# Kernel tuning notes

Measured on AMD Instinct MI355X. Metric: run time of the kernel, lower is better.

Reference implementation:

```python
import jax, jax.numpy as jnp
import numpy as np

N_NODES = 50000
N_EDGES = 800000
N_GRAPHS = 64
HEADS = 4
IN_CH, HID_CH, OUT_CH = 128, 64, 32


def setup_inputs() -> dict:
    key = jax.random.key(0)
    ks = jax.random.split(key, 13)
    x = jax.random.normal(ks[0], (N_NODES, IN_CH), dtype=jnp.float32)
    edge_index = jax.random.randint(ks[1], (2, N_EDGES), 0, N_NODES, dtype=jnp.int64)
    tensor_batch = jnp.sort(jax.random.randint(ks[2], (N_NODES,), 0, N_GRAPHS, dtype=jnp.int64))
    s = 0.1
    return {
        "x": x,
        "edge_index": edge_index,
        "tensor_batch": tensor_batch,
        "W1": jax.random.normal(ks[3], (IN_CH, HEADS * HID_CH), dtype=jnp.float32) * s,
        "a_src1": jax.random.normal(ks[4], (HEADS, HID_CH), dtype=jnp.float32) * s,
        "a_dst1": jax.random.normal(ks[5], (HEADS, HID_CH), dtype=jnp.float32) * s,
        "b1": jnp.zeros((HEADS * HID_CH,), dtype=jnp.float32),
        "W2": jax.random.normal(ks[6], (HEADS * HID_CH, HEADS * OUT_CH), dtype=jnp.float32) * s,
        "a_src2": jax.random.normal(ks[7], (HEADS, OUT_CH), dtype=jnp.float32) * s,
        "a_dst2": jax.random.normal(ks[8], (HEADS, OUT_CH), dtype=jnp.float32) * s,
        "b2": jnp.zeros((HEADS * OUT_CH,), dtype=jnp.float32),
        "Wout": jax.random.normal(ks[9], (HEADS * OUT_CH, 2), dtype=jnp.float32) * s,
        "bout": jnp.zeros((2,), dtype=jnp.float32),
    }


def gat_conv(x, src, dst, W, a_src, a_dst, b, heads, ch):
    """PyG-style GATConv (eval mode, self-loops already appended)."""
    N = x.shape[0]
    h = (x @ W).reshape(N, heads, ch)            # [N,H,C] per-head projection
    s = jnp.sum(h * a_src, axis=-1)              # [N,H] source attention term
    d = jnp.sum(h * a_dst, axis=-1)              # [N,H] dest attention term
    e = jax.nn.leaky_relu(s[src] + d[dst], negative_slope=0.2)   # [E,H]
    # segment softmax over incoming edges of each destination node
    m = jax.ops.segment_max(e, dst, num_segments=N)              # [N,H]
    ex = jnp.exp(e - m[dst])
    denom = jax.ops.segment_sum(ex, dst, num_segments=N)         # [N,H]
    alpha = ex / (denom[dst] + 1e-16)                            # [E,H]
    out = jax.ops.segment_sum(h[src] * alpha[:, :, None], dst, num_segments=N)
    return out.reshape(N, heads * ch) + b


def reference(x, edge_index, tensor_batch, W1, a_src1, a_dst1, b1,
              W2, a_src2, a_dst2, b2, Wout, bout):
    N = x.shape[0]
    loop = jnp.arange(N, dtype=edge_index.dtype)
    src = jnp.concatenate([edge_index[0], loop])  # add self-loops (PyG default)
    dst = jnp.concatenate([edge_index[1], loop])
    h = jax.nn.relu(gat_conv(x, src, dst, W1, a_src1, a_dst1, b1, HEADS, HID_CH))
    h = jax.nn.relu(gat_conv(h, src, dst, W2, a_src2, a_dst2, b2, HEADS, OUT_CH))
    # global mean pool per graph
    sums = jax.ops.segment_sum(h, tensor_batch, num_segments=N_GRAPHS)
    counts = jax.ops.segment_sum(jnp.ones((N, 1), h.dtype), tensor_batch, num_segments=N_GRAPHS)
    pooled = sums / jnp.maximum(counts, 1.0)
    logits = pooled @ Wout + bout
    return jax.nn.softmax(logits, axis=-1)
```

## Files before the change

kernel.cpp:

```cpp
#include <hip/hip_runtime.h>
#include <hip/hip_bf16.h>

#define N_NODES 50000
#define N_EDGES 800000
#define N_GRAPHS 64
#define HEADS 4
#define IN_CH 128
#define HID 64
#define F1 256
#define OUT_CH 32
#define F2 128
#define POOL_SPLITS 16
#define SCAN_B 256
#define SCAN_NB ((N_NODES + SCAN_B - 1) / SCAN_B)
#define GEMM_GRID ((N_NODES + 63) / 64)
#define COUNT_GRID ((N_EDGES + 255) / 256)
#define SCATTER_GRID ((N_EDGES / 4 + 255) / 256)

typedef unsigned short ushortT;
typedef unsigned int uintT;
typedef short v8s __attribute__((ext_vector_type(8)));
typedef float v4f __attribute__((ext_vector_type(4)));
typedef float v2f __attribute__((ext_vector_type(2)));

__device__ __forceinline__ ushortT f2bf(float f) {
    union { float f; unsigned int i; } v; v.f = f;
    unsigned int x = v.i;
    unsigned int r = (x + 0x7fffu + ((x >> 16) & 1u)) >> 16;
    return (ushortT)r;
}
__device__ __forceinline__ float bf_lo(uintT w) {
    union { unsigned int i; float f; } v; v.i = w << 16; return v.f;
}
__device__ __forceinline__ float bf_hi(uintT w) {
    union { unsigned int i; float f; } v; v.i = w & 0xffff0000u; return v.f;
}
__device__ __forceinline__ unsigned char f2fp8(float f) {
    return (unsigned char)__builtin_amdgcn_cvt_pk_fp8_f32(f, f, 0u, false);
}
__device__ __forceinline__ void fp8x4_acc(uintT w, float ex, float* acc) {
    v2f p0 = __builtin_amdgcn_cvt_pk_f32_fp8(w, false);
    v2f p1 = __builtin_amdgcn_cvt_pk_f32_fp8(w, true);
    acc[0] += ex * p0.x; acc[1] += ex * p0.y;
    acc[2] += ex * p1.x; acc[3] += ex * p1.y;
}

__device__ __forceinline__ void packW_one(const float* __restrict__ W,
                                          uint4* __restrict__ dst,
                                          int i, int FIN, int FOUT) {
    int KC = FIN / 32;
    int lane = i & 63, g = i >> 6;
    int kc = g % KC, nt = g / KC;
    int n = nt * 16 + (lane & 15);
    int kbase = kc * 32 + (lane >> 4) * 8;
    union { uint4 q; ushortT u[8]; } pk;
#pragma unroll
    for (int j = 0; j < 8; j++) pk.u[j] = f2bf(W[(kbase + j) * FOUT + n]);
    dst[i] = pk.q;
}

__global__ __launch_bounds__(256) void k_packw(
        const float* __restrict__ W1, const float* __restrict__ W2,
        uint4* __restrict__ wpk, int* __restrict__ counts) {
    int i = blockIdx.x * 256 + threadIdx.x;
    if (i < 4096) packW_one(W1, wpk, i, IN_CH, F1);
    else          packW_one(W2, wpk + 4096, i - 4096, F1, F2);
    for (int j = i; j < N_NODES; j += 8192) counts[j] = 0;
}

template <int FIN, int FOUT, bool ABF16>
__device__ __forceinline__ void gemm_body(const void* __restrict__ A,
                                          const uint4* __restrict__ Wpk,
                                          const float* __restrict__ ASrc,
                                          const float* __restrict__ ADst,
                                          unsigned char* __restrict__ out,
                                          float* __restrict__ s_out_g,
                                          float* __restrict__ d_out_g,
                                          int nrows, int bid) {
    constexpr int KC = FIN / 32;
    constexpr int NT = FOUT / 16;
    constexpr int NTH = (FOUT / HEADS) / 16;
    int tid = threadIdx.x;
    int wave = tid >> 6, lane = tid & 63;
    long row0 = (long)bid * 64 + wave * 16;
    if (row0 >= nrows) return;
    int m = lane & 15, b = lane >> 4;

    v8s af[KC];
    if (ABF16) {
        const ushortT* Ab = (const ushortT*)A;
#pragma unroll
        for (int kc = 0; kc < KC; kc++) {
            union { v8s v; uint4 q; } u;
            u.q = *(const uint4*)(Ab + (row0 + m) * FIN + kc * 32 + b * 8);
            af[kc] = u.v;
        }
    } else {
        const float* Af = (const float*)A;
#pragma unroll
        for (int kc = 0; kc < KC; kc++) {
            union { v8s v; ushortT u[8]; } u;
            const float* p = Af + (row0 + m) * FIN + kc * 32 + b * 8;
#pragma unroll
            for (int j = 0; j < 8; j++) u.u[j] = f2bf(p[j]);
            af[kc] = u.v;
        }
    }

    float sp[4] = {0,0,0,0}, dp[4] = {0,0,0,0};
    float sk[4], dk[4];
#pragma unroll
    for (int nt = 0; nt < NT; nt++) {
        v4f c = {0.f, 0.f, 0.f, 0.f};
#pragma unroll
        for (int kc = 0; kc < KC; kc++) {
            union { v8s v; uint4 q; } bu;
            bu.q = Wpk[(nt * KC + kc) * 64 + lane];
            c = __builtin_amdgcn_mfma_f32_16x16x32_bf16(af[kc], bu.v, c, 0, 0, 0);
        }
        int col = nt * 16 + m;
        float av = ASrc[col], dv = ADst[col];
        long r0 = row0 + b * 4;
#pragma unroll
        for (int reg = 0; reg < 4; reg++) {
            out[(r0 + reg) * FOUT + col] = f2fp8(c[reg]);
            sp[reg] += c[reg] * av;
            dp[reg] += c[reg] * dv;
        }
        if ((nt % NTH) == NTH - 1) {
#pragma unroll
            for (int o = 1; o < 16; o <<= 1) {
#pragma unroll
                for (int reg = 0; reg < 4; reg++) {
                    sp[reg] += __shfl_xor(sp[reg], o, 64);
                    dp[reg] += __shfl_xor(dp[reg], o, 64);
                }
            }
            int hd = nt / NTH;
#pragma unroll
            for (int reg = 0; reg < 4; reg++) {
                if (m == hd) { sk[reg] = sp[reg]; dk[reg] = dp[reg]; }
                sp[reg] = 0.f; dp[reg] = 0.f;
            }
        }
    }
    if (m < HEADS) {
        long r0 = row0 + b * 4;
#pragma unroll
        for (int reg = 0; reg < 4; reg++) {
            s_out_g[(r0 + reg) * HEADS + m] = sk[reg];
            d_out_g[(r0 + reg) * HEADS + m] = dk[reg];
        }
    }
}

__global__ __launch_bounds__(256) void k_mega1(
        const float* __restrict__ x, const uint4* __restrict__ wpk,
        const float* __restrict__ asrc1, const float* __restrict__ adst1,
        unsigned char* __restrict__ u_h, float* __restrict__ f_s,
        float* __restrict__ f_d, const int* __restrict__ ei,
        int* __restrict__ counts, int* __restrict__ rank) {
    if (blockIdx.x < GEMM_GRID) {
        gemm_body<IN_CH, F1, false>(x, wpk, asrc1, adst1, u_h, f_s, f_d,
                                    N_NODES, blockIdx.x);
    } else {
        int e = (blockIdx.x - GEMM_GRID) * 256 + threadIdx.x;
        if (e < N_EDGES) {
            int dst = ei[N_EDGES + e];
            rank[e] = atomicAdd(&counts[dst], 1);
        }
    }
}

__global__ __launch_bounds__(256) void k_gemm2(
        const ushortT* __restrict__ A, const uint4* __restrict__ wpk2,
        const float* __restrict__ asrc2, const float* __restrict__ adst2,
        unsigned char* __restrict__ u_h, float* __restrict__ f_s,
        float* __restrict__ f_d) {
    gemm_body<F1, F2, true>(A, wpk2, asrc2, adst2, u_h, f_s, f_d,
                            N_NODES, blockIdx.x);
}

__global__ void k_scan1(const int* __restrict__ counts, int* __restrict__ offs,
                        int* __restrict__ bsum) {
    __shared__ int sh[SCAN_B];
    int b = blockIdx.x, t = threadIdx.x;
    int i = b * SCAN_B + t;
    int v = (i < N_NODES) ? counts[i] : 0;
    sh[t] = v;
    __syncthreads();
    for (int o = 1; o < SCAN_B; o <<= 1) {
        int add = (t >= o) ? sh[t - o] : 0;
        __syncthreads();
        sh[t] += add;
        __syncthreads();
    }
    if (i < N_NODES) offs[i] = sh[t] - v;
    if (t == SCAN_B - 1) bsum[b] = sh[t];
}

__global__ void k_scan2(const int* __restrict__ bsum, int* __restrict__ bbase,
                        int* __restrict__ offs, const int* __restrict__ batch,
                        int* __restrict__ bounds) {
    __shared__ int sh[SCAN_B];
    int t = threadIdx.x;
    int v = (t < SCAN_NB) ? bsum[t] : 0;
    sh[t] = v;
    __syncthreads();
    for (int o = 1; o < SCAN_B; o <<= 1) {
        int add = (t >= o) ? sh[t - o] : 0;
        __syncthreads();
        sh[t] += add;
        __syncthreads();
    }
    if (t < SCAN_NB) bbase[t] = sh[t] - v;
    if (t == SCAN_B - 1) offs[N_NODES] = sh[t];
    if (t <= N_GRAPHS) {
        int lo = 0, hi = N_NODES;
        while (lo < hi) {
            int mid = (lo + hi) >> 1;
            if (batch[mid] < t) lo = mid + 1; else hi = mid;
        }
        bounds[t] = lo;
    }
}

__global__ __launch_bounds__(256) void k_scatter(
        const int* __restrict__ ei, const int* __restrict__ offs,
        const int* __restrict__ bbase, const int* __restrict__ rank,
        int* __restrict__ csr_src) {
    int e4 = (blockIdx.x * 256 + threadIdx.x) * 4;
    if (e4 >= N_EDGES) return;
    int4 src = *(const int4*)(ei + e4);
    int4 dst = *(const int4*)(ei + N_EDGES + e4);
    int4 rk  = *(const int4*)(rank + e4);
    csr_src[offs[dst.x] + bbase[dst.x >> 8] + rk.x] = src.x;
    csr_src[offs[dst.y] + bbase[dst.y >> 8] + rk.y] = src.y;
    csr_src[offs[dst.z] + bbase[dst.z >> 8] + rk.z] = src.z;
    csr_src[offs[dst.w] + bbase[dst.w >> 8] + rk.w] = src.w;
}

template <int C, int VEC, int WPB, int CHUNK>
__global__ __launch_bounds__(64 * WPB) void k_agg(
        const unsigned char* __restrict__ hb, const float* __restrict__ s,
        const float* __restrict__ d, const int* __restrict__ offs,
        const int* __restrict__ bbase, const int* __restrict__ csr_src,
        const float* __restrict__ bias, ushortT* __restrict__ xout) {
    constexpr int F = HEADS * C;
    constexpr int TPN = F / VEC;
    static_assert(TPN == 16, "four nodes per wave");
    static_assert(C / VEC == 4, "head = tl>>2");
    static_assert(N_NODES % (WPB * 4) == 0, "exact grid");
    __shared__ int lsrc[WPB][4][CHUNK];
    __shared__ float lex[WPB][4][CHUNK * HEADS];
    int wv = threadIdx.x >> 6;
    int t = threadIdx.x & 63;
    int q = t >> 4, tl = t & 15;
    int n = (blockIdx.x * WPB + wv) * 4 + q;
    int h = tl >> 2;
    int beg = offs[n] + bbase[n >> 8];
    int np1 = n + 1;
    int end = (np1 < N_NODES) ? offs[np1] + bbase[np1 >> 8] : offs[N_NODES];
    float4 dn = *(const float4*)(d + n * 4);

    float4 svn = *(const float4*)(s + n * 4);
    float ssel = (h == 0) ? svn.x : (h == 1) ? svn.y : (h == 2) ? svn.z : svn.w;
    float dsel = (h == 0) ? dn.x : (h == 1) ? dn.y : (h == 2) ? dn.z : dn.w;
    float es = ssel + dsel; es = es > 0.f ? es : 0.2f * es;
    float exs = __expf(es);
    float sumex = exs;
    float acc[VEC];
#pragma unroll
    for (int j = 0; j < VEC; j++) acc[j] = 0.f;
    if (VEC == 16) {
        uint4 w = ((const uint4*)hb)[(long)n * TPN + tl];
        fp8x4_acc(w.x, exs, acc);      fp8x4_acc(w.y, exs, acc + 4);
        fp8x4_acc(w.z, exs, acc + 8);  fp8x4_acc(w.w, exs, acc + 12);
    } else {
        uint2 w = ((const uint2*)hb)[(long)n * TPN + tl];
        fp8x4_acc(w.x, exs, acc);      fp8x4_acc(w.y, exs, acc + 4);
    }

    int tot = end - beg;
    int m1 = max(tot, __shfl_xor(tot, 16, 64));
    int maxTot = max(m1, __shfl_xor(m1, 32, 64));
    for (int base = 0; base < maxTot; base += CHUNK) {
        int cnt = min(CHUNK, tot - base); if (cnt < 0) cnt = 0;
        int cntW = min(CHUNK, maxTot - base);
        for (int i = tl; i < cnt; i += TPN) {
            int sn = csr_src[beg + base + i];
            lsrc[wv][q][i] = sn;
            float4 sv = *(const float4*)(s + sn * 4);
            float e0 = sv.x + dn.x; e0 = e0 > 0.f ? e0 : 0.2f * e0;
            float e1 = sv.y + dn.y; e1 = e1 > 0.f ? e1 : 0.2f * e1;
            float e2 = sv.z + dn.z; e2 = e2 > 0.f ? e2 : 0.2f * e2;
            float e3 = sv.w + dn.w; e3 = e3 > 0.f ? e3 : 0.2f * e3;
            float4 exv = { __expf(e0), __expf(e1), __expf(e2), __expf(e3) };
            *(float4*)&lex[wv][q][i * 4] = exv;
        }
        asm volatile("s_waitcnt lgkmcnt(0)" ::: "memory");
#pragma unroll 4
        for (int i = 0; i < cntW; i++) {
            bool act = i < cnt;
            float ex = act ? lex[wv][q][i * 4 + h] : 0.f;
            int sn = act ? lsrc[wv][q][i] : 0;
            sumex += ex;
            if (VEC == 16) {
                uint4 w = ((const uint4*)hb)[(long)sn * TPN + tl];
                fp8x4_acc(w.x, ex, acc);      fp8x4_acc(w.y, ex, acc + 4);
                fp8x4_acc(w.z, ex, acc + 8);  fp8x4_acc(w.w, ex, acc + 12);
            } else {
                uint2 w = ((const uint2*)hb)[(long)sn * TPN + tl];
                fp8x4_acc(w.x, ex, acc);      fp8x4_acc(w.y, ex, acc + 4);
            }
        }
        asm volatile("" ::: "memory");
    }
    float inv = 1.f / (sumex + 1e-16f);
    float o[VEC];
#pragma unroll
    for (int j = 0; j < VEC; j++)
        o[j] = fmaxf(acc[j] * inv + bias[tl * VEC + j], 0.f);
    if (VEC == 16) {
        uint4 pk0, pk1;
        pk0.x = (uintT)f2bf(o[0])  | ((uintT)f2bf(o[1])  << 16);
        pk0.y = (uintT)f2bf(o[2])  | ((uintT)f2bf(o[3])  << 16);
        pk0.z = (uintT)f2bf(o[4])  | ((uintT)f2bf(o[5])  << 16);
        pk0.w = (uintT)f2bf(o[6])  | ((uintT)f2bf(o[7])  << 16);
        pk1.x = (uintT)f2bf(o[8])  | ((uintT)f2bf(o[9])  << 16);
        pk1.y = (uintT)f2bf(o[10]) | ((uintT)f2bf(o[11]) << 16);
        pk1.z = (uintT)f2bf(o[12]) | ((uintT)f2bf(o[13]) << 16);
        pk1.w = (uintT)f2bf(o[14]) | ((uintT)f2bf(o[15]) << 16);
        long u4base = ((long)n * TPN + tl) * 2;
        ((uint4*)xout)[u4base + 0] = pk0;
        ((uint4*)xout)[u4base + 1] = pk1;
    } else {
        uint4 pk;
        pk.x = (uintT)f2bf(o[0]) | ((uintT)f2bf(o[1]) << 16);
        pk.y = (uintT)f2bf(o[2]) | ((uintT)f2bf(o[3]) << 16);
        pk.z = (uintT)f2bf(o[4]) | ((uintT)f2bf(o[5]) << 16);
        pk.w = (uintT)f2bf(o[6]) | ((uintT)f2bf(o[7]) << 16);
        ((uint4*)xout)[(long)n * TPN + tl] = pk;
    }
}

__global__ void k_pool_partial(const ushortT* __restrict__ x2, const int* __restrict__ bounds,
                               float* __restrict__ partial) {
    int g = blockIdx.x, s = blockIdx.y;
    int t = threadIdx.x;
    int half = t >> 6, tl = t & 63;
    int n0 = bounds[g], n1 = bounds[g + 1];
    int len = n1 - n0;
    int a = n0 + (int)((long)len * s / POOL_SPLITS);
    int b = n0 + (int)((long)len * (s + 1) / POOL_SPLITS);
    float a0 = 0.f, a1 = 0.f;
    const uintT* x2u = (const uintT*)x2;
    for (int n = a + half; n < b; n += 2) {
        uintT w = x2u[(long)n * 64 + tl];
        a0 += bf_lo(w); a1 += bf_hi(w);
    }
    float2 pr = {a0, a1};
    *(float2*)&partial[(((long)g * 2 * POOL_SPLITS) + (s * 2 + half)) * F2 + 2 * tl] = pr;
}

__global__ void k_head(const float* __restrict__ partial, const int* __restrict__ bounds,
                       const float* __restrict__ Wout, const float* __restrict__ bout,
                       float* __restrict__ out) {
    __shared__ float red0[F2], red1[F2];
    int g = blockIdx.x;
    int t = threadIdx.x;
    int cntN = bounds[g + 1] - bounds[g];
    float cnt = fmaxf((float)cntN, 1.0f);
    float sum = 0.f;
    for (int s = 0; s < 2 * POOL_SPLITS; s++)
        sum += partial[((long)g * 2 * POOL_SPLITS + s) * F2 + t];
    float p = sum / cnt;
    red0[t] = p * Wout[t * 2 + 0];
    red1[t] = p * Wout[t * 2 + 1];
    __syncthreads();
    for (int off = F2 / 2; off > 0; off >>= 1) {
        if (t < off) { red0[t] += red0[t + off]; red1[t] += red1[t + off]; }
        __syncthreads();
    }
    if (t == 0) {
        float l0 = red0[0] + bout[0];
        float l1 = red1[0] + bout[1];
        float m = fmaxf(l0, l1);
        float e0 = __expf(l0 - m), e1 = __expf(l1 - m);
        float inv = 1.f / (e0 + e1);
        out[g * 2 + 0] = e0 * inv;
        out[g * 2 + 1] = e1 * inv;
    }
}

extern "C" void kernel_launch(void* const* d_in, const int* in_sizes, int n_in,
                              void* d_out, int out_size, void* d_ws, size_t ws_size,
                              hipStream_t stream) {
    const float* x     = (const float*)d_in[0];
    const int*   ei    = (const int*)d_in[1];
    const int*   batch = (const int*)d_in[2];
    const float* W1    = (const float*)d_in[3];
    const float* asrc1 = (const float*)d_in[4];
    const float* adst1 = (const float*)d_in[5];
    const float* b1    = (const float*)d_in[6];
    const float* W2    = (const float*)d_in[7];
    const float* asrc2 = (const float*)d_in[8];
    const float* adst2 = (const float*)d_in[9];
    const float* b2    = (const float*)d_in[10];
    const float* Wout  = (const float*)d_in[11];
    const float* bout  = (const float*)d_in[12];

    char* ws = (char*)d_ws;
    size_t off = 0;
    auto alloc = [&](size_t bytes) -> void* {
        void* p = ws + off;
        off += (bytes + 255) / 256 * 256;
        return p;
    };
    unsigned char* u_h = (unsigned char*)alloc((size_t)N_NODES * F1);
    ushortT* u_x1  = (ushortT*)alloc(sizeof(ushortT) * (size_t)N_NODES * F1);
    ushortT* u_x2  = (ushortT*)alloc(sizeof(ushortT) * (size_t)N_NODES * F2);
    uint4*   wpk   = (uint4*)alloc(sizeof(uint4) * 8192);
    float*   f_s   = (float*)alloc(sizeof(float) * (size_t)N_NODES * HEADS);
    float*   f_d   = (float*)alloc(sizeof(float) * (size_t)N_NODES * HEADS);
    int*     i_cnt = (int*)alloc(sizeof(int) * (size_t)N_NODES);
    int*     i_off = (int*)alloc(sizeof(int) * (size_t)(N_NODES + 1));
    int*     i_rnk = (int*)alloc(sizeof(int) * (size_t)N_EDGES);
    int*     i_csr = (int*)alloc(sizeof(int) * (size_t)N_EDGES);
    int*     i_bnd = (int*)alloc(sizeof(int) * (size_t)(N_GRAPHS + 1));
    int*     i_bs  = (int*)alloc(sizeof(int) * SCAN_NB);
    int*     i_bb  = (int*)alloc(sizeof(int) * SCAN_NB);
    float*   f_prt = (float*)alloc(sizeof(float) * (size_t)N_GRAPHS * 2 * POOL_SPLITS * F2);
    (void)ws_size; (void)in_sizes; (void)n_in; (void)out_size;

    k_packw<<<32, 256, 0, stream>>>(W1, W2, wpk, i_cnt);

    k_mega1<<<GEMM_GRID + COUNT_GRID, 256, 0, stream>>>(
        x, wpk, asrc1, adst1, u_h, f_s, f_d, ei, i_cnt, i_rnk);

    k_scan1<<<SCAN_NB, SCAN_B, 0, stream>>>(i_cnt, i_off, i_bs);
    k_scan2<<<1, SCAN_B, 0, stream>>>(i_bs, i_bb, i_off, batch, i_bnd);
    k_scatter<<<SCATTER_GRID, 256, 0, stream>>>(ei, i_off, i_bb, i_rnk, i_csr);

    int agg_grid = N_NODES / (4 * 4);

    k_agg<HID, 16, 4, 64><<<agg_grid, 256, 0, stream>>>(
        u_h, f_s, f_d, i_off, i_bb, i_csr, b1, u_x1);

    k_gemm2<<<GEMM_GRID, 256, 0, stream>>>(u_x1, wpk + 4096, asrc2, adst2,
                                           u_h, f_s, f_d);
    k_agg<OUT_CH, 8, 4, 64><<<agg_grid, 256, 0, stream>>>(
        u_h, f_s, f_d, i_off, i_bb, i_csr, b2, u_x2);

    dim3 pgrid(N_GRAPHS, POOL_SPLITS);
    k_pool_partial<<<pgrid, F2, 0, stream>>>(u_x2, i_bnd, f_prt);
    k_head<<<N_GRAPHS, F2, 0, stream>>>(f_prt, i_bnd, Wout, bout, (float*)d_out);
}
```

Baseline: 246.6 us.

## Fuse layer-1 aggregation with layer-2 GEMM through shared memory

Adds a k_aggemm kernel that does the layer-1 attention aggregation for 16 nodes per block, writes the bf16 results into padded shared memory, and then runs the layer-2 MFMA projection and attention-score reductions on that tile. This removes the global round trip of the 50000x256 bf16 intermediate and one kernel launch. Layer-2 outputs go to separate buffers (u_h2, f_s2, f_d2) so the fused kernel does not overwrite layer-1 data other blocks are still reading. The cost is a larger block footprint (more shared memory and registers), which may lower occupancy for the gather-bound aggregation, and a small 16-row GEMM tile per block.

```diff
diff --git a/kernel.cpp b/kernel.cpp
--- a/kernel.cpp
+++ b/kernel.cpp
@@ -16,6 +16,8 @@
 #define GEMM_GRID ((N_NODES + 63) / 64)
 #define COUNT_GRID ((N_EDGES + 255) / 256)
 #define SCATTER_GRID ((N_EDGES / 4 + 255) / 256)
+#define AGEMM_GRID (N_NODES / 16)
+#define HPAD 264
 
 typedef unsigned short ushortT;
 typedef unsigned int uintT;
@@ -68,43 +70,31 @@
     for (int j = i; j < N_NODES; j += 8192) counts[j] = 0;
 }
 
-template <int FIN, int FOUT, bool ABF16>
-__device__ __forceinline__ void gemm_body(const void* __restrict__ A,
-                                          const uint4* __restrict__ Wpk,
-                                          const float* __restrict__ ASrc,
-                                          const float* __restrict__ ADst,
-                                          unsigned char* __restrict__ out,
-                                          float* __restrict__ s_out_g,
-                                          float* __restrict__ d_out_g,
-                                          int nrows, int bid) {
-    constexpr int KC = FIN / 32;
-    constexpr int NT = FOUT / 16;
-    constexpr int NTH = (FOUT / HEADS) / 16;
+__device__ __forceinline__ void gemm1_body(const float* __restrict__ A,
+                                           const uint4* __restrict__ Wpk,
+                                           const float* __restrict__ ASrc,
+                                           const float* __restrict__ ADst,
+                                           unsigned char* __restrict__ out,
+                                           float* __restrict__ s_out_g,
+                                           float* __restrict__ d_out_g,
+                                           int bid) {
+    constexpr int KC = IN_CH / 32;
+    constexpr int NT = F1 / 16;
+    constexpr int NTH = (F1 / HEADS) / 16;
     int tid = threadIdx.x;
     int wave = tid >> 6, lane = tid & 63;
     long row0 = (long)bid * 64 + wave * 16;
-    if (row0 >= nrows) return;
+    if (row0 >= N_NODES) return;
     int m = lane & 15, b = lane >> 4;
 
     v8s af[KC];
-    if (ABF16) {
-        const ushortT* Ab = (const ushortT*)A;
-#pragma unroll
-        for (int kc = 0; kc < KC; kc++) {
-            union { v8s v; uint4 q; } u;
-            u.q = *(const uint4*)(Ab + (row0 + m) * FIN + kc * 32 + b * 8);
-            af[kc] = u.v;
-        }
-    } else {
-        const float* Af = (const float*)A;
-#pragma unroll
-        for (int kc = 0; kc < KC; kc++) {
-            union { v8s v; ushortT u[8]; } u;
-            const float* p = Af + (row0 + m) * FIN + kc * 32 + b * 8;
-#pragma unroll
-            for (int j = 0; j < 8; j++) u.u[j] = f2bf(p[j]);
-            af[kc] = u.v;
-        }
+#pragma unroll
+    for (int kc = 0; kc < KC; kc++) {
+        union { v8s v; ushortT u[8]; } u;
+        const float* p = A + (row0 + m) * IN_CH + kc * 32 + b * 8;
+#pragma unroll
+        for (int j = 0; j < 8; j++) u.u[j] = f2bf(p[j]);
+        af[kc] = u.v;
     }
 
     float sp[4] = {0,0,0,0}, dp[4] = {0,0,0,0};
@@ -123,7 +113,7 @@
         long r0 = row0 + b * 4;
 #pragma unroll
         for (int reg = 0; reg < 4; reg++) {
-            out[(r0 + reg) * FOUT + col] = f2fp8(c[reg]);
+            out[(r0 + reg) * F1 + col] = f2fp8(c[reg]);
             sp[reg] += c[reg] * av;
             dp[reg] += c[reg] * dv;
         }
@@ -161,8 +151,7 @@
         float* __restrict__ f_d, const int* __restrict__ ei,
         int* __restrict__ counts, int* __restrict__ rank) {
     if (blockIdx.x < GEMM_GRID) {
-        gemm_body<IN_CH, F1, false>(x, wpk, asrc1, adst1, u_h, f_s, f_d,
-                                    N_NODES, blockIdx.x);
+        gemm1_body(x, wpk, asrc1, adst1, u_h, f_s, f_d, blockIdx.x);
     } else {
         int e = (blockIdx.x - GEMM_GRID) * 256 + threadIdx.x;
         if (e < N_EDGES) {
@@ -170,15 +159,6 @@
             rank[e] = atomicAdd(&counts[dst], 1);
         }
     }
-}
-
-__global__ __launch_bounds__(256) void k_gemm2(
-        const ushortT* __restrict__ A, const uint4* __restrict__ wpk2,
-        const float* __restrict__ asrc2, const float* __restrict__ adst2,
-        unsigned char* __restrict__ u_h, float* __restrict__ f_s,
-        float* __restrict__ f_d) {
-    gemm_body<F1, F2, true>(A, wpk2, asrc2, adst2, u_h, f_s, f_d,
-                            N_NODES, blockIdx.x);
 }
 
 __global__ void k_scan1(const int* __restrict__ counts, int* __restrict__ offs,
@@ -238,6 +218,144 @@
     csr_src[offs[dst.y] + bbase[dst.y >> 8] + rk.y] = src.y;
     csr_src[offs[dst.z] + bbase[dst.z >> 8] + rk.z] = src.z;
     csr_src[offs[dst.w] + bbase[dst.w >> 8] + rk.w] = src.w;
+}
+
+__global__ __launch_bounds__(256) void k_aggemm(
+        const unsigned char* __restrict__ hb, const float* __restrict__ s,
+        const float* __restrict__ d, const int* __restrict__ offs,
+        const int* __restrict__ bbase, const int* __restrict__ csr_src,
+        const float* __restrict__ b1, const uint4* __restrict__ wpk2,
+        const float* __restrict__ asrc2, const float* __restrict__ adst2,
+        unsigned char* __restrict__ h2, float* __restrict__ s2,
+        float* __restrict__ d2) {
+    constexpr int CHUNK = 32;
+    constexpr int TPN = 16;
+    __shared__ int lsrc[4][4][CHUNK];
+    __shared__ float lex[4][4][CHUNK * HEADS];
+    __shared__ ushortT lh[16 * HPAD];
+    int wv = threadIdx.x >> 6;
+    int t = threadIdx.x & 63;
+    int q = t >> 4, tl = t & 15;
+    int nloc = wv * 4 + q;
+    int n = blockIdx.x * 16 + nloc;
+    int h = tl >> 2;
+    int beg = offs[n] + bbase[n >> 8];
+    int np1 = n + 1;
+    int end = (np1 < N_NODES) ? offs[np1] + bbase[np1 >> 8] : offs[N_NODES];
+    float4 dn = *(const float4*)(d + n * 4);
+
+    float4 svn = *(const float4*)(s + n * 4);
+    float ssel = (h == 0) ? svn.x : (h == 1) ? svn.y : (h == 2) ? svn.z : svn.w;
+    float dsel = (h == 0) ? dn.x : (h == 1) ? dn.y : (h == 2) ? dn.z : dn.w;
+    float es = ssel + dsel; es = es > 0.f ? es : 0.2f * es;
+    float exs = __expf(es);
+    float sumex = exs;
+    float acc[16];
+#pragma unroll
+    for (int j = 0; j < 16; j++) acc[j] = 0.f;
+    {
+        uint4 w = ((const uint4*)hb)[(long)n * TPN + tl];
+        fp8x4_acc(w.x, exs, acc);      fp8x4_acc(w.y, exs, acc + 4);
+        fp8x4_acc(w.z, exs, acc + 8);  fp8x4_acc(w.w, exs, acc + 12);
+    }
+
+    int tot = end - beg;
+    int m1 = max(tot, __shfl_xor(tot, 16, 64));
+    int maxTot = max(m1, __shfl_xor(m1, 32, 64));
+    for (int base = 0; base < maxTot; base += CHUNK) {
+        int cnt = min(CHUNK, tot - base); if (cnt < 0) cnt = 0;
+        int cntW = min(CHUNK, maxTot - base);
+        for (int i = tl; i < cnt; i += TPN) {
+            int sn = csr_src[beg + base + i];
+            lsrc[wv][q][i] = sn;
+            float4 sv = *(const float4*)(s + sn * 4);
+            float e0 = sv.x + dn.x; e0 = e0 > 0.f ? e0 : 0.2f * e0;
+            float e1 = sv.y + dn.y; e1 = e1 > 0.f ? e1 : 0.2f * e1;
+            float e2 = sv.z + dn.z; e2 = e2 > 0.f ? e2 : 0.2f * e2;
+            float e3 = sv.w + dn.w; e3 = e3 > 0.f ? e3 : 0.2f * e3;
+            float4 exv = { __expf(e0), __expf(e1), __expf(e2), __expf(e3) };
+            *(float4*)&lex[wv][q][i * 4] = exv;
+        }
+        asm volatile("s_waitcnt lgkmcnt(0)" ::: "memory");
+#pragma unroll 4
+        for (int i = 0; i < cntW; i++) {
+            bool act = i < cnt;
+            float ex = act ? lex[wv][q][i * 4 + h] : 0.f;
+            int sn = act ? lsrc[wv][q][i] : 0;
+            sumex += ex;
+            uint4 w = ((const uint4*)hb)[(long)sn * TPN + tl];
+            fp8x4_acc(w.x, ex, acc);      fp8x4_acc(w.y, ex, acc + 4);
+            fp8x4_acc(w.z, ex, acc + 8);  fp8x4_acc(w.w, ex, acc + 12);
+        }
+        asm volatile("" ::: "memory");
+    }
+    float inv = 1.f / (sumex + 1e-16f);
+    float o[16];
+#pragma unroll
+    for (int j = 0; j < 16; j++)
+        o[j] = fmaxf(acc[j] * inv + b1[tl * 16 + j], 0.f);
+    uint4 pk0, pk1;
+    pk0.x = (uintT)f2bf(o[0])  | ((uintT)f2bf(o[1])  << 16);
+    pk0.y = (uintT)f2bf(o[2])  | ((uintT)f2bf(o[3])  << 16);
+    pk0.z = (uintT)f2bf(o[4])  | ((uintT)f2bf(o[5])  << 16);
+    pk0.w = (uintT)f2bf(o[6])  | ((uintT)f2bf(o[7])  << 16);
+    pk1.x = (uintT)f2bf(o[8])  | ((uintT)f2bf(o[9])  << 16);
+    pk1.y = (uintT)f2bf(o[10]) | ((uintT)f2bf(o[11]) << 16);
+    pk1.z = (uintT)f2bf(o[12]) | ((uintT)f2bf(o[13]) << 16);
+    pk1.w = (uintT)f2bf(o[14]) | ((uintT)f2bf(o[15]) << 16);
+    *(uint4*)&lh[nloc * HPAD + tl * 16]     = pk0;
+    *(uint4*)&lh[nloc * HPAD + tl * 16 + 8] = pk1;
+    __syncthreads();
+
+    constexpr int KC = F1 / 32;
+    constexpr int NTH2 = (F2 / HEADS) / 16;
+    int wave = wv, lane = t;
+    int m = lane & 15, b = lane >> 4;
+    long row0 = (long)blockIdx.x * 16;
+
+    v8s af[KC];
+#pragma unroll
+    for (int kc = 0; kc < KC; kc++) {
+        union { v8s v; uint4 q; } u;
+        u.q = *(const uint4*)&lh[m * HPAD + kc * 32 + b * 8];
+        af[kc] = u.v;
+    }
+
+    float sp[4] = {0,0,0,0}, dp[4] = {0,0,0,0};
+#pragma unroll
+    for (int j = 0; j < NTH2; j++) {
+        int nt = wave * NTH2 + j;
+        v4f c = {0.f, 0.f, 0.f, 0.f};
+#pragma unroll
+        for (int kc = 0; kc < KC; kc++) {
+            union { v8s v; uint4 q; } bu;
+            bu.q = wpk2[(nt * KC + kc) * 64 + lane];
+            c = __builtin_amdgcn_mfma_f32_16x16x32_bf16(af[kc], bu.v, c, 0, 0, 0);
+        }
+        int col = nt * 16 + m;
+        float av = asrc2[col], dv = adst2[col];
+#pragma unroll
+        for (int reg = 0; reg < 4; reg++) {
+            h2[(row0 + b * 4 + reg) * F2 + col] = f2fp8(c[reg]);
+            sp[reg] += c[reg] * av;
+            dp[reg] += c[reg] * dv;
+        }
+    }
+#pragma unroll
+    for (int o2 = 1; o2 < 16; o2 <<= 1) {
+#pragma unroll
+        for (int reg = 0; reg < 4; reg++) {
+            sp[reg] += __shfl_xor(sp[reg], o2, 64);
+            dp[reg] += __shfl_xor(dp[reg], o2, 64);
+        }
+    }
+    if (m == 0) {
+#pragma unroll
+        for (int reg = 0; reg < 4; reg++) {
+            s2[(row0 + b * 4 + reg) * HEADS + wave] = sp[reg];
+            d2[(row0 + b * 4 + reg) * HEADS + wave] = dp[reg];
+        }
+    }
 }
 
 template <int C, int VEC, int WPB, int CHUNK>
@@ -272,11 +390,7 @@
     float acc[VEC];
 #pragma unroll
     for (int j = 0; j < VEC; j++) acc[j] = 0.f;
-    if (VEC == 16) {
-        uint4 w = ((const uint4*)hb)[(long)n * TPN + tl];
-        fp8x4_acc(w.x, exs, acc);      fp8x4_acc(w.y, exs, acc + 4);
-        fp8x4_acc(w.z, exs, acc + 8);  fp8x4_acc(w.w, exs, acc + 12);
-    } else {
+    {
         uint2 w = ((const uint2*)hb)[(long)n * TPN + tl];
         fp8x4_acc(w.x, exs, acc);      fp8x4_acc(w.y, exs, acc + 4);
     }
@@ -305,14 +419,8 @@
             float ex = act ? lex[wv][q][i * 4 + h] : 0.f;
             int sn = act ? lsrc[wv][q][i] : 0;
             sumex += ex;
-            if (VEC == 16) {
-                uint4 w = ((const uint4*)hb)[(long)sn * TPN + tl];
-                fp8x4_acc(w.x, ex, acc);      fp8x4_acc(w.y, ex, acc + 4);
-                fp8x4_acc(w.z, ex, acc + 8);  fp8x4_acc(w.w, ex, acc + 12);
-            } else {
-                uint2 w = ((const uint2*)hb)[(long)sn * TPN + tl];
-                fp8x4_acc(w.x, ex, acc);      fp8x4_acc(w.y, ex, acc + 4);
-            }
+            uint2 w = ((const uint2*)hb)[(long)sn * TPN + tl];
+            fp8x4_acc(w.x, ex, acc);      fp8x4_acc(w.y, ex, acc + 4);
         }
         asm volatile("" ::: "memory");
     }
@@ -321,27 +429,12 @@
 #pragma unroll
     for (int j = 0; j < VEC; j++)
         o[j] = fmaxf(acc[j] * inv + bias[tl * VEC + j], 0.f);
-    if (VEC == 16) {
-        uint4 pk0, pk1;
-        pk0.x = (uintT)f2bf(o[0])  | ((uintT)f2bf(o[1])  << 16);
-        pk0.y = (uintT)f2bf(o[2])  | ((uintT)f2bf(o[3])  << 16);
-        pk0.z = (uintT)f2bf(o[4])  | ((uintT)f2bf(o[5])  << 16);
-        pk0.w = (uintT)f2bf(o[6])  | ((uintT)f2bf(o[7])  << 16);
-        pk1.x = (uintT)f2bf(o[8])  | ((uintT)f2bf(o[9])  << 16);
-        pk1.y = (uintT)f2bf(o[10]) | ((uintT)f2bf(o[11]) << 16);
-        pk1.z = (uintT)f2bf(o[12]) | ((uintT)f2bf(o[13]) << 16);
-        pk1.w = (uintT)f2bf(o[14]) | ((uintT)f2bf(o[15]) << 16);
-        long u4base = ((long)n * TPN + tl) * 2;
-        ((uint4*)xout)[u4base + 0] = pk0;
-        ((uint4*)xout)[u4base + 1] = pk1;
-    } else {
-        uint4 pk;
-        pk.x = (uintT)f2bf(o[0]) | ((uintT)f2bf(o[1]) << 16);
-        pk.y = (uintT)f2bf(o[2]) | ((uintT)f2bf(o[3]) << 16);
-        pk.z = (uintT)f2bf(o[4]) | ((uintT)f2bf(o[5]) << 16);
-        pk.w = (uintT)f2bf(o[6]) | ((uintT)f2bf(o[7]) << 16);
-        ((uint4*)xout)[(long)n * TPN + tl] = pk;
-    }
+    uint4 pk;
+    pk.x = (uintT)f2bf(o[0]) | ((uintT)f2bf(o[1]) << 16);
+    pk.y = (uintT)f2bf(o[2]) | ((uintT)f2bf(o[3]) << 16);
+    pk.z = (uintT)f2bf(o[4]) | ((uintT)f2bf(o[5]) << 16);
+    pk.w = (uintT)f2bf(o[6]) | ((uintT)f2bf(o[7]) << 16);
+    ((uint4*)xout)[(long)n * TPN + tl] = pk;
 }
 
 __global__ void k_pool_partial(const ushortT* __restrict__ x2, const int* __restrict__ bounds,
@@ -418,11 +511,13 @@
         return p;
     };
     unsigned char* u_h = (unsigned char*)alloc((size_t)N_NODES * F1);
-    ushortT* u_x1  = (ushortT*)alloc(sizeof(ushortT) * (size_t)N_NODES * F1);
+    unsigned char* u_h2 = (unsigned char*)alloc((size_t)N_NODES * F2);
     ushortT* u_x2  = (ushortT*)alloc(sizeof(ushortT) * (size_t)N_NODES * F2);
     uint4*   wpk   = (uint4*)alloc(sizeof(uint4) * 8192);
     float*   f_s   = (float*)alloc(sizeof(float) * (size_t)N_NODES * HEADS);
     float*   f_d   = (float*)alloc(sizeof(float) * (size_t)N_NODES * HEADS);
+    float*   f_s2  = (float*)alloc(sizeof(float) * (size_t)N_NODES * HEADS);
+    float*   f_d2  = (float*)alloc(sizeof(float) * (size_t)N_NODES * HEADS);
     int*     i_cnt = (int*)alloc(sizeof(int) * (size_t)N_NODES);
     int*     i_off = (int*)alloc(sizeof(int) * (size_t)(N_NODES + 1));
     int*     i_rnk = (int*)alloc(sizeof(int) * (size_t)N_EDGES);
@@ -442,15 +537,13 @@
     k_scan2<<<1, SCAN_B, 0, stream>>>(i_bs, i_bb, i_off, batch, i_bnd);
     k_scatter<<<SCATTER_GRID, 256, 0, stream>>>(ei, i_off, i_bb, i_rnk, i_csr);
 
+    k_aggemm<<<AGEMM_GRID, 256, 0, stream>>>(
+        u_h, f_s, f_d, i_off, i_bb, i_csr, b1, wpk + 4096, asrc2, adst2,
+        u_h2, f_s2, f_d2);
+
     int agg_grid = N_NODES / (4 * 4);
-
-    k_agg<HID, 16, 4, 64><<<agg_grid, 256, 0, stream>>>(
-        u_h, f_s, f_d, i_off, i_bb, i_csr, b1, u_x1);
-
-    k_gemm2<<<GEMM_GRID, 256, 0, stream>>>(u_x1, wpk + 4096, asrc2, adst2,
-                                           u_h, f_s, f_d);
     k_agg<OUT_CH, 8, 4, 64><<<agg_grid, 256, 0, stream>>>(
-        u_h, f_s, f_d, i_off, i_bb, i_csr, b2, u_x2);
+        u_h2, f_s2, f_d2, i_off, i_bb, i_csr, b2, u_x2);
 
     dim3 pgrid(N_GRAPHS, POOL_SPLITS);
     k_pool_partial<<<pgrid, F2, 0, stream>>>(u_x2, i_bnd, f_prt);
```

After: 238.2 us (median of 2 runs). -3.4%, faster.
